# Performance work log

Measured on AMD Instinct MI355X. Metric: run time of the kernel, lower is better.

The kernel has to match this reference:

```python
import jax, jax.numpy as jnp
import numpy as np

B = 64         # number of hypernetwork samples (scenes)
N = 16384      # number of query points
SIZE_IN = 256
SIZE_H = 128
SIZE_OUT = 128


def setup_inputs() -> dict:
    key = jax.random.key(0)
    k0, k1, k2, k3, k4, k5, k6 = jax.random.split(key, 7)
    # scale weights like small init to keep activations sane
    kls0 = jax.random.normal(k0, (B, SIZE_H, SIZE_IN), dtype=jnp.float32) * 0.05
    kls1 = jax.random.normal(k1, (B, SIZE_OUT, SIZE_H), dtype=jnp.float32) * 0.05
    kls2 = jax.random.normal(k2, (B, SIZE_OUT, SIZE_IN), dtype=jnp.float32) * 0.05
    bias0 = jax.random.normal(k3, (B, SIZE_H), dtype=jnp.float32) * 0.05
    bias1 = jax.random.normal(k4, (B, SIZE_OUT), dtype=jnp.float32) * 0.05
    x = jax.random.normal(k5, (N, SIZE_IN), dtype=jnp.float32)
    batch_index = jax.random.randint(k6, (N,), 0, B, dtype=jnp.int64)
    return {
        "kls0": kls0, "kls1": kls1, "kls2": kls2,
        "bias0": bias0, "bias1": bias1,
        "x": x, "batch_index": batch_index,
    }


def reference(kls0, kls1, kls2, bias0, bias1, x, batch_index):
    bi = batch_index
    # net = F.linear(relu(x), kls0[bi], bias0[bi])  -> per-row GEMV with gathered weights
    net = jnp.einsum("nhi,ni->nh", kls0[bi], jax.nn.relu(x)) + bias0[bi]
    # dx = F.linear(relu(net), kls1[bi], bias1[bi])
    dx = jnp.einsum("noh,nh->no", kls1[bi], jax.nn.relu(net)) + bias1[bi]
    # shortcut (size_in != size_out): x_s = F.linear(x, kls2[bi])
    x_s = jnp.einsum("noi,ni->no", kls2[bi], x)
    return x_s + dx
```

## Files before the change

kernel.cpp:

```cpp
#include <hip/hip_runtime.h>

#define NSCENE 64
#define NPTS   16384
#define SIN    256
#define SH     128
#define SOUT   128
#define TILE_P 32

#define WS_PARTIAL 0
#define WS_OFFSETS 16384
#define WS_PERM    17408
#define WS_WBF16   82944
#define W0_ELEMS   (NSCENE*SH*SIN)
#define W1_ELEMS   (NSCENE*SOUT*SH)
#define W2_ELEMS   (NSCENE*SOUT*SIN)
#define WTOT       (W0_ELEMS+W1_ELEMS+W2_ELEMS)
#define CONV_BLOCKS (WTOT/2048)

typedef __attribute__((ext_vector_type(8))) short bf16x8;
typedef __attribute__((ext_vector_type(4))) float f32x4;

__device__ __forceinline__ short f2bf(float f) {
  unsigned int u = __float_as_uint(f);
  unsigned int r = (u + 0x7FFFu + ((u >> 16) & 1u)) >> 16;
  return (short)(r & 0xFFFFu);
}

__device__ __forceinline__ bf16x8 cvt8(const float* src) {
  float4 u0 = *reinterpret_cast<const float4*>(src);
  float4 u1 = *reinterpret_cast<const float4*>(src + 4);
  return (bf16x8){f2bf(u0.x), f2bf(u0.y), f2bf(u0.z), f2bf(u0.w),
                  f2bf(u1.x), f2bf(u1.y), f2bf(u1.z), f2bf(u1.w)};
}


__global__ __launch_bounds__(256) void prep_kernel(
    const int* __restrict__ bidx,
    const float* __restrict__ kls0, const float* __restrict__ kls1,
    const float* __restrict__ kls2,
    int* __restrict__ partial, short* __restrict__ wb)
{
  int b = blockIdx.x;
  int tid = threadIdx.x;
  if (b < 64) {
    __shared__ int lh[NSCENE];
    if (tid < NSCENE) lh[tid] = 0;
    __syncthreads();
    atomicAdd(&lh[bidx[b * 256 + tid]], 1);
    __syncthreads();
    if (tid < NSCENE) partial[b * 64 + tid] = lh[tid];
  } else {
    int e = ((b - 64) * 256 + tid) * 8;
    if (e < WTOT) {
      const float* src;
      if (e < W0_ELEMS) {
        int s = e >> 15, r = e & 32767;
        int w = r >> 12, ks = (r >> 9) & 7, l = (r >> 3) & 63;
        int row = w * 16 + (l & 15), k = ks * 32 + (l >> 4) * 8;
        src = kls0 + ((size_t)s << 15) + row * SIN + k;
      } else if (e < W0_ELEMS + W1_ELEMS) {
        int e1 = e - W0_ELEMS;
        int s = e1 >> 14, r = e1 & 16383;
        int w = r >> 11, ks = (r >> 9) & 3, l = (r >> 3) & 63;
        int row = w * 16 + (l & 15), k = ks * 32 + (l >> 4) * 8;
        src = kls1 + ((size_t)s << 14) + row * SH + k;
      } else {
        int e2 = e - W0_ELEMS - W1_ELEMS;
        int s = e2 >> 15, r = e2 & 32767;
        int w = r >> 12, ks = (r >> 9) & 7, l = (r >> 3) & 63;
        int row = w * 16 + (l & 15), k = ks * 32 + (l >> 4) * 8;
        src = kls2 + ((size_t)s << 15) + row * SIN + k;
      }
      *reinterpret_cast<bf16x8*>(wb + e) = cvt8(src);
    }
  }
}


__global__ __launch_bounds__(256) void scatter_kernel(
    const int* __restrict__ bidx, const int* __restrict__ partial,
    int* __restrict__ offsets, int* __restrict__ perm)
{
  __shared__ int cur[NSCENE];
  int b = blockIdx.x;
  int tid = threadIdx.x;
  if (tid < 64) {
    int s = tid;
    int colpre = 0, total = 0;
    for (int bb = 0; bb < 64; ++bb) {
      int v = partial[bb * 64 + s];
      if (bb < b) colpre += v;
      total += v;
    }
    int v = total;
    for (int off = 1; off < 64; off <<= 1) {
      int t = __shfl_up(v, off);
      if (s >= off) v += t;
    }
    int sceneoff = v - total;
    cur[s] = sceneoff + colpre;
    if (b == 0) {
      offsets[s] = sceneoff;
      if (s == 63) offsets[64] = NPTS;
    }
  }
  __syncthreads();
  int n = b * 256 + tid;
  int s = bidx[n];
  int pos = atomicAdd(&cur[s], 1);
  perm[pos] = n;
}


__global__ __launch_bounds__(512) void fused_kernel(
    const float* __restrict__ bias0, const float* __restrict__ bias1,
    const float* __restrict__ x,
    const int* __restrict__ offsets, const int* __restrict__ perm,
    const short* __restrict__ wb, float* __restrict__ out)
{
  __shared__ __align__(16) short xr[TILE_P][SIN + 8];
  __shared__ __align__(16) short xp[TILE_P][SIN + 8];
  __shared__ __align__(16) short snet[TILE_P][SH + 8];
  __shared__ int ptile[TILE_P];

  const int s    = blockIdx.x & 63;
  const int t0   = blockIdx.x >> 6;
  const int base = offsets[s];
  const int cnt  = offsets[s + 1] - base;
  const int tid  = threadIdx.x;
  const int lane = tid & 63;
  const int w    = tid >> 6;
  const int l15  = lane & 15;
  const int lh4  = lane >> 4;
  const int col  = w * 16 + l15;

  const short* B0s = wb + ((size_t)s << 15) + (w << 12) + (lane << 3);
  const short* B1s = wb + W0_ELEMS + ((size_t)s << 14) + (w << 11) + (lane << 3);
  const short* B2s = wb + W0_ELEMS + W1_ELEMS + ((size_t)s << 15) + (w << 12) + (lane << 3);

  const float bv0 = bias0[(size_t)s * SH + col];
  const float bv1 = bias1[(size_t)s * SOUT + col];

  bf16x8 b0c[8], b2c[8], b1c[4];
#pragma unroll
  for (int ks = 0; ks < 8; ++ks) {
    b0c[ks] = *reinterpret_cast<const bf16x8*>(B0s + (ks << 9));
    b2c[ks] = *reinterpret_cast<const bf16x8*>(B2s + (ks << 9));
  }
#pragma unroll
  for (int ks = 0; ks < 4; ++ks)
    b1c[ks] = *reinterpret_cast<const bf16x8*>(B1s + (ks << 9));

  for (int t = t0; t * TILE_P < cnt; t += 8) {
    __syncthreads();

    {
      int r  = tid >> 4;
      int cg = tid & 15;
      int prow = t * TILE_P + r;
      int np = (prow < cnt) ? perm[base + prow] : -1;
      if (cg == 0) ptile[r] = np;
      const float* xrow = x + (size_t)(np < 0 ? 0 : np) * SIN;
      int c0 = cg * 16;
      for (int j = 0; j < 16; j += 4) {
        float4 v = make_float4(0.f, 0.f, 0.f, 0.f);
        if (np >= 0) v = *reinterpret_cast<const float4*>(xrow + c0 + j);
        short4 p, q;
        p.x = f2bf(v.x); p.y = f2bf(v.y); p.z = f2bf(v.z); p.w = f2bf(v.w);
        q.x = f2bf(fmaxf(v.x, 0.f)); q.y = f2bf(fmaxf(v.y, 0.f));
        q.z = f2bf(fmaxf(v.z, 0.f)); q.w = f2bf(fmaxf(v.w, 0.f));
        *reinterpret_cast<short4*>(&xp[r][c0 + j]) = p;
        *reinterpret_cast<short4*>(&xr[r][c0 + j]) = q;
      }
    }
    __syncthreads();

    f32x4 acc0[2], acc[2];
#pragma unroll
    for (int mt = 0; mt < 2; ++mt) {
      acc0[mt] = (f32x4){bv0, bv0, bv0, bv0};
      acc[mt]  = (f32x4){bv1, bv1, bv1, bv1};
    }
#pragma unroll
    for (int ks = 0; ks < 8; ++ks) {
      int kc = ks * 32 + lh4 * 8;
#pragma unroll
      for (int mt = 0; mt < 2; ++mt) {
        bf16x8 aR = *reinterpret_cast<const bf16x8*>(&xr[mt * 16 + l15][kc]);
        bf16x8 aP = *reinterpret_cast<const bf16x8*>(&xp[mt * 16 + l15][kc]);
        acc0[mt] = __builtin_amdgcn_mfma_f32_16x16x32_bf16(aR, b0c[ks], acc0[mt], 0, 0, 0);
        acc[mt]  = __builtin_amdgcn_mfma_f32_16x16x32_bf16(aP, b2c[ks], acc[mt],  0, 0, 0);
      }
    }

#pragma unroll
    for (int mt = 0; mt < 2; ++mt)
#pragma unroll
      for (int r4 = 0; r4 < 4; ++r4)
        snet[mt * 16 + lh4 * 4 + r4][col] = f2bf(fmaxf(acc0[mt][r4], 0.f));
    __syncthreads();

#pragma unroll
    for (int ks = 0; ks < 4; ++ks) {
      int kc = ks * 32 + lh4 * 8;
#pragma unroll
      for (int mt = 0; mt < 2; ++mt) {
        bf16x8 aS = *reinterpret_cast<const bf16x8*>(&snet[mt * 16 + l15][kc]);
        acc[mt] = __builtin_amdgcn_mfma_f32_16x16x32_bf16(aS, b1c[ks], acc[mt], 0, 0, 0);
      }
    }

#pragma unroll
    for (int mt = 0; mt < 2; ++mt)
#pragma unroll
      for (int r4 = 0; r4 < 4; ++r4) {
        int row = mt * 16 + lh4 * 4 + r4;
        int pt = ptile[row];
        if (pt >= 0) out[(size_t)pt * SOUT + col] = acc[mt][r4];
      }
  }
}


extern "C" void kernel_launch(void* const* d_in, const int* in_sizes, int n_in,
                              void* d_out, int out_size, void* d_ws, size_t ws_size,
                              hipStream_t stream) {
  const float* kls0  = (const float*)d_in[0];
  const float* kls1  = (const float*)d_in[1];
  const float* kls2  = (const float*)d_in[2];
  const float* bias0 = (const float*)d_in[3];
  const float* bias1 = (const float*)d_in[4];
  const float* x     = (const float*)d_in[5];
  const int*   bidx  = (const int*)d_in[6];
  float* out = (float*)d_out;

  int*   partial = (int*)((char*)d_ws + WS_PARTIAL);
  int*   offsets = (int*)((char*)d_ws + WS_OFFSETS);
  int*   perm    = (int*)((char*)d_ws + WS_PERM);
  short* wb      = (short*)((char*)d_ws + WS_WBF16);

  prep_kernel<<<64 + CONV_BLOCKS, 256, 0, stream>>>(
      bidx, kls0, kls1, kls2, partial, wb);
  scatter_kernel<<<64, 256, 0, stream>>>(bidx, partial, offsets, perm);
  fused_kernel<<<512, 512, 0, stream>>>(bias0, bias1, x, offsets, perm, wb, out);
}
```

Before: 28.76 us.

## Pre-gather x into MFMA fragment layout and stream weights from global

Adds a separate gather kernel that converts x rows, in scene-sorted order padded to 32-row tiles, into bf16 fragment-ordered buffers for both the relu and raw paths. The fused kernel then reads A fragments straight from global memory instead of staging through LDS. It uses 256-thread blocks where each wave computes two column tiles, loads weight fragments per k-step rather than caching them in registers, and grows the grid to 768 blocks. The aim is to drop the LDS staging and conversion from the hot loop and raise occupancy, at the cost of an extra kernel launch and an extra round trip of x through global memory.

```diff
diff --git a/kernel.cpp b/kernel.cpp
--- a/kernel.cpp
+++ b/kernel.cpp
@@ -5,17 +5,19 @@
 #define SIN    256
 #define SH     128
 #define SOUT   128
-#define TILE_P 32
+#define XSLOTS 18432
 
 #define WS_PARTIAL 0
 #define WS_OFFSETS 16384
-#define WS_PERM    17408
-#define WS_WBF16   82944
+#define WS_SLOTMAP 17408
+#define WS_WBF16   (17408 + 73728)
+#define WS_XG      (WS_WBF16 + 10485760)
 #define W0_ELEMS   (NSCENE*SH*SIN)
 #define W1_ELEMS   (NSCENE*SOUT*SH)
 #define W2_ELEMS   (NSCENE*SOUT*SIN)
 #define WTOT       (W0_ELEMS+W1_ELEMS+W2_ELEMS)
 #define CONV_BLOCKS (WTOT/2048)
+#define XR_ELEMS   (XSLOTS * 256)
 
 typedef __attribute__((ext_vector_type(8))) short bf16x8;
 typedef __attribute__((ext_vector_type(4))) float f32x4;
@@ -55,20 +57,20 @@
       const float* src;
       if (e < W0_ELEMS) {
         int s = e >> 15, r = e & 32767;
-        int w = r >> 12, ks = (r >> 9) & 7, l = (r >> 3) & 63;
-        int row = w * 16 + (l & 15), k = ks * 32 + (l >> 4) * 8;
+        int cg = r >> 12, ks = (r >> 9) & 7, l = (r >> 3) & 63;
+        int row = cg * 16 + (l & 15), k = ks * 32 + (l >> 4) * 8;
         src = kls0 + ((size_t)s << 15) + row * SIN + k;
       } else if (e < W0_ELEMS + W1_ELEMS) {
         int e1 = e - W0_ELEMS;
         int s = e1 >> 14, r = e1 & 16383;
-        int w = r >> 11, ks = (r >> 9) & 3, l = (r >> 3) & 63;
-        int row = w * 16 + (l & 15), k = ks * 32 + (l >> 4) * 8;
+        int cg = r >> 11, ks = (r >> 9) & 3, l = (r >> 3) & 63;
+        int row = cg * 16 + (l & 15), k = ks * 32 + (l >> 4) * 8;
         src = kls1 + ((size_t)s << 14) + row * SH + k;
       } else {
         int e2 = e - W0_ELEMS - W1_ELEMS;
         int s = e2 >> 15, r = e2 & 32767;
-        int w = r >> 12, ks = (r >> 9) & 7, l = (r >> 3) & 63;
-        int row = w * 16 + (l & 15), k = ks * 32 + (l >> 4) * 8;
+        int cg = r >> 12, ks = (r >> 9) & 7, l = (r >> 3) & 63;
+        int row = cg * 16 + (l & 15), k = ks * 32 + (l >> 4) * 8;
         src = kls2 + ((size_t)s << 15) + row * SIN + k;
       }
       *reinterpret_cast<bf16x8*>(wb + e) = cvt8(src);
@@ -79,9 +81,10 @@
 
 __global__ __launch_bounds__(256) void scatter_kernel(
     const int* __restrict__ bidx, const int* __restrict__ partial,
-    int* __restrict__ offsets, int* __restrict__ perm)
+    int* __restrict__ offsets, int* __restrict__ slotmap)
 {
   __shared__ int cur[NSCENE];
+  __shared__ int scnt[NSCENE], soff[NSCENE];
   int b = blockIdx.x;
   int tid = threadIdx.x;
   if (tid < 64) {
@@ -92,121 +95,154 @@
       if (bb < b) colpre += v;
       total += v;
     }
-    int v = total;
+    int p = (total + 31) & ~31;
+    int v = p;
     for (int off = 1; off < 64; off <<= 1) {
       int t = __shfl_up(v, off);
       if (s >= off) v += t;
     }
-    int sceneoff = v - total;
-    cur[s] = sceneoff + colpre;
+    int offp = v - p;
+    cur[s]  = offp + colpre;
+    scnt[s] = total;
+    soff[s] = offp;
     if (b == 0) {
-      offsets[s] = sceneoff;
-      if (s == 63) offsets[64] = NPTS;
+      offsets[s] = offp;
+      if (s == 63) offsets[64] = v;
     }
   }
   __syncthreads();
+  if (b == 0 && tid < 64) {
+    int st = soff[tid] + scnt[tid];
+    int en = soff[tid] + ((scnt[tid] + 31) & ~31);
+    for (int i = st; i < en; ++i) slotmap[i] = -1;
+  }
   int n = b * 256 + tid;
-  int s = bidx[n];
-  int pos = atomicAdd(&cur[s], 1);
-  perm[pos] = n;
-}
-
-
-__global__ __launch_bounds__(512) void fused_kernel(
+  int s2 = bidx[n];
+  int pos = atomicAdd(&cur[s2], 1);
+  slotmap[pos] = n;
+}
+
+
+__global__ __launch_bounds__(256) void xgather_kernel(
+    const float* __restrict__ x, const int* __restrict__ slotmap,
+    short* __restrict__ xg)
+{
+  int slot = blockIdx.x * 32 + (threadIdx.x >> 3);
+  int ks   = threadIdx.x & 7;
+  int n = slotmap[slot];
+  if ((unsigned)n >= (unsigned)NPTS) return;
+  const float* px = x + (size_t)n * SIN + ks * 32;
+  size_t fo = ((size_t)(slot >> 4) << 12) + (ks << 9) + ((slot & 15) << 3);
+  short* xr = xg + fo;
+  short* xp = xg + XR_ELEMS + fo;
+#pragma unroll
+  for (int h4 = 0; h4 < 4; ++h4) {
+    float4 u0 = *reinterpret_cast<const float4*>(px + h4 * 8);
+    float4 u1 = *reinterpret_cast<const float4*>(px + h4 * 8 + 4);
+    bf16x8 vp = (bf16x8){f2bf(u0.x), f2bf(u0.y), f2bf(u0.z), f2bf(u0.w),
+                         f2bf(u1.x), f2bf(u1.y), f2bf(u1.z), f2bf(u1.w)};
+    bf16x8 vr = (bf16x8){f2bf(fmaxf(u0.x, 0.f)), f2bf(fmaxf(u0.y, 0.f)),
+                         f2bf(fmaxf(u0.z, 0.f)), f2bf(fmaxf(u0.w, 0.f)),
+                         f2bf(fmaxf(u1.x, 0.f)), f2bf(fmaxf(u1.y, 0.f)),
+                         f2bf(fmaxf(u1.z, 0.f)), f2bf(fmaxf(u1.w, 0.f))};
+    *reinterpret_cast<bf16x8*>(xp + h4 * 128) = vp;
+    *reinterpret_cast<bf16x8*>(xr + h4 * 128) = vr;
+  }
+}
+
+
+__global__ __launch_bounds__(256, 4) void fused_kernel(
     const float* __restrict__ bias0, const float* __restrict__ bias1,
-    const float* __restrict__ x,
-    const int* __restrict__ offsets, const int* __restrict__ perm,
-    const short* __restrict__ wb, float* __restrict__ out)
-{
-  __shared__ __align__(16) short xr[TILE_P][SIN + 8];
-  __shared__ __align__(16) short xp[TILE_P][SIN + 8];
-  __shared__ __align__(16) short snet[TILE_P][SH + 8];
-  __shared__ int ptile[TILE_P];
-
-  const int s    = blockIdx.x & 63;
-  const int t0   = blockIdx.x >> 6;
-  const int base = offsets[s];
-  const int cnt  = offsets[s + 1] - base;
-  const int tid  = threadIdx.x;
-  const int lane = tid & 63;
-  const int w    = tid >> 6;
-  const int l15  = lane & 15;
-  const int lh4  = lane >> 4;
-  const int col  = w * 16 + l15;
-
-  const short* B0s = wb + ((size_t)s << 15) + (w << 12) + (lane << 3);
-  const short* B1s = wb + W0_ELEMS + ((size_t)s << 14) + (w << 11) + (lane << 3);
-  const short* B2s = wb + W0_ELEMS + W1_ELEMS + ((size_t)s << 15) + (w << 12) + (lane << 3);
-
-  const float bv0 = bias0[(size_t)s * SH + col];
-  const float bv1 = bias1[(size_t)s * SOUT + col];
-
-  bf16x8 b0c[8], b2c[8], b1c[4];
-#pragma unroll
-  for (int ks = 0; ks < 8; ++ks) {
-    b0c[ks] = *reinterpret_cast<const bf16x8*>(B0s + (ks << 9));
-    b2c[ks] = *reinterpret_cast<const bf16x8*>(B2s + (ks << 9));
-  }
-#pragma unroll
-  for (int ks = 0; ks < 4; ++ks)
-    b1c[ks] = *reinterpret_cast<const bf16x8*>(B1s + (ks << 9));
-
-  for (int t = t0; t * TILE_P < cnt; t += 8) {
-    __syncthreads();
-
-    {
-      int r  = tid >> 4;
-      int cg = tid & 15;
-      int prow = t * TILE_P + r;
-      int np = (prow < cnt) ? perm[base + prow] : -1;
-      if (cg == 0) ptile[r] = np;
-      const float* xrow = x + (size_t)(np < 0 ? 0 : np) * SIN;
-      int c0 = cg * 16;
-      for (int j = 0; j < 16; j += 4) {
-        float4 v = make_float4(0.f, 0.f, 0.f, 0.f);
-        if (np >= 0) v = *reinterpret_cast<const float4*>(xrow + c0 + j);
-        short4 p, q;
-        p.x = f2bf(v.x); p.y = f2bf(v.y); p.z = f2bf(v.z); p.w = f2bf(v.w);
-        q.x = f2bf(fmaxf(v.x, 0.f)); q.y = f2bf(fmaxf(v.y, 0.f));
-        q.z = f2bf(fmaxf(v.z, 0.f)); q.w = f2bf(fmaxf(v.w, 0.f));
-        *reinterpret_cast<short4*>(&xp[r][c0 + j]) = p;
-        *reinterpret_cast<short4*>(&xr[r][c0 + j]) = q;
-      }
-    }
-    __syncthreads();
-
-    f32x4 acc0[2], acc[2];
-#pragma unroll
-    for (int mt = 0; mt < 2; ++mt) {
-      acc0[mt] = (f32x4){bv0, bv0, bv0, bv0};
-      acc[mt]  = (f32x4){bv1, bv1, bv1, bv1};
-    }
+    const int* __restrict__ offsets, const int* __restrict__ slotmap,
+    const short* __restrict__ wb, const short* __restrict__ xg,
+    float* __restrict__ out)
+{
+  __shared__ __align__(16) short snet[32][SH + 8];
+
+  const int s     = blockIdx.x & 63;
+  const int tslot = blockIdx.x >> 6;
+  const int base  = offsets[s];
+  const int cntp  = offsets[s + 1] - base;
+  const int tid   = threadIdx.x;
+  const int lane  = tid & 63;
+  const int w     = tid >> 6;
+  const int l15   = lane & 15;
+  const int lh4   = lane >> 4;
+
+  const short* wb0 = wb + ((size_t)s << 15);
+  const short* wb1 = wb + W0_ELEMS + ((size_t)s << 14);
+  const short* wb2 = wb + W0_ELEMS + W1_ELEMS + ((size_t)s << 15);
+  const short* xr  = xg;
+  const short* xp  = xg + XR_ELEMS;
+
+  float bv0[2], bv1[2];
+#pragma unroll
+  for (int nt = 0; nt < 2; ++nt) {
+    int col = (2 * w + nt) * 16 + l15;
+    bv0[nt] = bias0[(size_t)s * SH + col];
+    bv1[nt] = bias1[(size_t)s * SOUT + col];
+  }
+
+  for (int t = tslot; t * 32 < cntp; t += 12) {
+    const int p0 = base + t * 32;
+    int ptv = (lane < 32) ? slotmap[p0 + lane] : -1;
+    const size_t xo = ((size_t)(p0 >> 4) << 12) + (lane << 3);
+    __syncthreads();
+
+    f32x4 acc0[2][2], acc1[2][2];
+#pragma unroll
+    for (int mt = 0; mt < 2; ++mt)
+#pragma unroll
+      for (int nt = 0; nt < 2; ++nt) {
+        acc0[mt][nt] = (f32x4){bv0[nt], bv0[nt], bv0[nt], bv0[nt]};
+        acc1[mt][nt] = (f32x4){bv1[nt], bv1[nt], bv1[nt], bv1[nt]};
+      }
+
 #pragma unroll
     for (int ks = 0; ks < 8; ++ks) {
-      int kc = ks * 32 + lh4 * 8;
+      bf16x8 aR[2], aP[2], b0f[2], b2f[2];
 #pragma unroll
       for (int mt = 0; mt < 2; ++mt) {
-        bf16x8 aR = *reinterpret_cast<const bf16x8*>(&xr[mt * 16 + l15][kc]);
-        bf16x8 aP = *reinterpret_cast<const bf16x8*>(&xp[mt * 16 + l15][kc]);
-        acc0[mt] = __builtin_amdgcn_mfma_f32_16x16x32_bf16(aR, b0c[ks], acc0[mt], 0, 0, 0);
-        acc[mt]  = __builtin_amdgcn_mfma_f32_16x16x32_bf16(aP, b2c[ks], acc[mt],  0, 0, 0);
-      }
+        aR[mt] = *reinterpret_cast<const bf16x8*>(xr + xo + ((size_t)mt << 12) + (ks << 9));
+        aP[mt] = *reinterpret_cast<const bf16x8*>(xp + xo + ((size_t)mt << 12) + (ks << 9));
+      }
+#pragma unroll
+      for (int nt = 0; nt < 2; ++nt) {
+        int fo = ((2 * w + nt) << 12) + (ks << 9) + (lane << 3);
+        b0f[nt] = *reinterpret_cast<const bf16x8*>(wb0 + fo);
+        b2f[nt] = *reinterpret_cast<const bf16x8*>(wb2 + fo);
+      }
+#pragma unroll
+      for (int mt = 0; mt < 2; ++mt)
+#pragma unroll
+        for (int nt = 0; nt < 2; ++nt) {
+          acc0[mt][nt] = __builtin_amdgcn_mfma_f32_16x16x32_bf16(aR[mt], b0f[nt], acc0[mt][nt], 0, 0, 0);
+          acc1[mt][nt] = __builtin_amdgcn_mfma_f32_16x16x32_bf16(aP[mt], b2f[nt], acc1[mt][nt], 0, 0, 0);
+        }
     }
 
 #pragma unroll
     for (int mt = 0; mt < 2; ++mt)
 #pragma unroll
-      for (int r4 = 0; r4 < 4; ++r4)
-        snet[mt * 16 + lh4 * 4 + r4][col] = f2bf(fmaxf(acc0[mt][r4], 0.f));
+      for (int nt = 0; nt < 2; ++nt)
+#pragma unroll
+        for (int r4 = 0; r4 < 4; ++r4)
+          snet[mt * 16 + lh4 * 4 + r4][(2 * w + nt) * 16 + l15] =
+              f2bf(fmaxf(acc0[mt][nt][r4], 0.f));
     __syncthreads();
 
 #pragma unroll
     for (int ks = 0; ks < 4; ++ks) {
-      int kc = ks * 32 + lh4 * 8;
+      bf16x8 b1f[2];
+#pragma unroll
+      for (int nt = 0; nt < 2; ++nt)
+        b1f[nt] = *reinterpret_cast<const bf16x8*>(wb1 + ((2 * w + nt) << 11) + (ks << 9) + (lane << 3));
 #pragma unroll
       for (int mt = 0; mt < 2; ++mt) {
-        bf16x8 aS = *reinterpret_cast<const bf16x8*>(&snet[mt * 16 + l15][kc]);
-        acc[mt] = __builtin_amdgcn_mfma_f32_16x16x32_bf16(aS, b1c[ks], acc[mt], 0, 0, 0);
+        bf16x8 aS = *reinterpret_cast<const bf16x8*>(&snet[mt * 16 + l15][ks * 32 + lh4 * 8]);
+#pragma unroll
+        for (int nt = 0; nt < 2; ++nt)
+          acc1[mt][nt] = __builtin_amdgcn_mfma_f32_16x16x32_bf16(aS, b1f[nt], acc1[mt][nt], 0, 0, 0);
       }
     }
 
@@ -215,8 +251,12 @@
 #pragma unroll
       for (int r4 = 0; r4 < 4; ++r4) {
         int row = mt * 16 + lh4 * 4 + r4;
-        int pt = ptile[row];
-        if (pt >= 0) out[(size_t)pt * SOUT + col] = acc[mt][r4];
+        int pt = __shfl(ptv, row);
+        if (pt >= 0) {
+#pragma unroll
+          for (int nt = 0; nt < 2; ++nt)
+            out[(size_t)pt * SOUT + (2 * w + nt) * 16 + l15] = acc1[mt][nt][r4];
+        }
       }
   }
 }
@@ -236,11 +276,13 @@
 
   int*   partial = (int*)((char*)d_ws + WS_PARTIAL);
   int*   offsets = (int*)((char*)d_ws + WS_OFFSETS);
-  int*   perm    = (int*)((char*)d_ws + WS_PERM);
+  int*   slotmap = (int*)((char*)d_ws + WS_SLOTMAP);
   short* wb      = (short*)((char*)d_ws + WS_WBF16);
+  short* xg      = (short*)((char*)d_ws + WS_XG);
 
   prep_kernel<<<64 + CONV_BLOCKS, 256, 0, stream>>>(
       bidx, kls0, kls1, kls2, partial, wb);
-  scatter_kernel<<<64, 256, 0, stream>>>(bidx, partial, offsets, perm);
-  fused_kernel<<<512, 512, 0, stream>>>(bias0, bias1, x, offsets, perm, wb, out);
-}
+  scatter_kernel<<<64, 256, 0, stream>>>(bidx, partial, offsets, slotmap);
+  xgather_kernel<<<XSLOTS / 32, 256, 0, stream>>>(x, slotmap, xg);
+  fused_kernel<<<768, 256, 0, stream>>>(bias0, bias1, offsets, slotmap, wb, xg, out);
+}
```

After: 61.32 us. +113.2%, slower.

## Fuse histogram, scatter and weight conversion into one per-scene kernel

Applied to the files above, without the earlier changes.

Replaces the three-kernel pipeline (histogram plus bf16 weight pre-conversion, scatter into a permutation, compute) with a single kernel. Each block scans the whole batch_index array to build its scene's point list in shared memory with a block-wide prefix sum. It converts its scene's fp32 weights to bf16 fragments directly in registers, so the workspace round trips and two kernel launches go away. The trade-off is that every block re-reads all of batch_index, and the weights are converted redundantly by the 8 blocks per scene. The list is capped at 768 points per scene, which assumes a roughly uniform scene distribution.

```diff
diff --git a/kernel.cpp b/kernel.cpp
--- a/kernel.cpp
+++ b/kernel.cpp
@@ -5,17 +5,7 @@
 #define SIN    256
 #define SH     128
 #define SOUT   128
-#define TILE_P 32
-
-#define WS_PARTIAL 0
-#define WS_OFFSETS 16384
-#define WS_PERM    17408
-#define WS_WBF16   82944
-#define W0_ELEMS   (NSCENE*SH*SIN)
-#define W1_ELEMS   (NSCENE*SOUT*SH)
-#define W2_ELEMS   (NSCENE*SOUT*SIN)
-#define WTOT       (W0_ELEMS+W1_ELEMS+W2_ELEMS)
-#define CONV_BLOCKS (WTOT/2048)
+#define MAXP   768
 
 typedef __attribute__((ext_vector_type(8))) short bf16x8;
 typedef __attribute__((ext_vector_type(4))) float f32x4;
@@ -34,99 +24,20 @@
 }
 
 
-__global__ __launch_bounds__(256) void prep_kernel(
-    const int* __restrict__ bidx,
+__global__ __launch_bounds__(512) void fused_all(
     const float* __restrict__ kls0, const float* __restrict__ kls1,
-    const float* __restrict__ kls2,
-    int* __restrict__ partial, short* __restrict__ wb)
+    const float* __restrict__ kls2, const float* __restrict__ bias0,
+    const float* __restrict__ bias1, const float* __restrict__ x,
+    const int* __restrict__ bidx, float* __restrict__ out)
 {
-  int b = blockIdx.x;
-  int tid = threadIdx.x;
-  if (b < 64) {
-    __shared__ int lh[NSCENE];
-    if (tid < NSCENE) lh[tid] = 0;
-    __syncthreads();
-    atomicAdd(&lh[bidx[b * 256 + tid]], 1);
-    __syncthreads();
-    if (tid < NSCENE) partial[b * 64 + tid] = lh[tid];
-  } else {
-    int e = ((b - 64) * 256 + tid) * 8;
-    if (e < WTOT) {
-      const float* src;
-      if (e < W0_ELEMS) {
-        int s = e >> 15, r = e & 32767;
-        int w = r >> 12, ks = (r >> 9) & 7, l = (r >> 3) & 63;
-        int row = w * 16 + (l & 15), k = ks * 32 + (l >> 4) * 8;
-        src = kls0 + ((size_t)s << 15) + row * SIN + k;
-      } else if (e < W0_ELEMS + W1_ELEMS) {
-        int e1 = e - W0_ELEMS;
-        int s = e1 >> 14, r = e1 & 16383;
-        int w = r >> 11, ks = (r >> 9) & 3, l = (r >> 3) & 63;
-        int row = w * 16 + (l & 15), k = ks * 32 + (l >> 4) * 8;
-        src = kls1 + ((size_t)s << 14) + row * SH + k;
-      } else {
-        int e2 = e - W0_ELEMS - W1_ELEMS;
-        int s = e2 >> 15, r = e2 & 32767;
-        int w = r >> 12, ks = (r >> 9) & 7, l = (r >> 3) & 63;
-        int row = w * 16 + (l & 15), k = ks * 32 + (l >> 4) * 8;
-        src = kls2 + ((size_t)s << 15) + row * SIN + k;
-      }
-      *reinterpret_cast<bf16x8*>(wb + e) = cvt8(src);
-    }
-  }
-}
-
-
-__global__ __launch_bounds__(256) void scatter_kernel(
-    const int* __restrict__ bidx, const int* __restrict__ partial,
-    int* __restrict__ offsets, int* __restrict__ perm)
-{
-  __shared__ int cur[NSCENE];
-  int b = blockIdx.x;
-  int tid = threadIdx.x;
-  if (tid < 64) {
-    int s = tid;
-    int colpre = 0, total = 0;
-    for (int bb = 0; bb < 64; ++bb) {
-      int v = partial[bb * 64 + s];
-      if (bb < b) colpre += v;
-      total += v;
-    }
-    int v = total;
-    for (int off = 1; off < 64; off <<= 1) {
-      int t = __shfl_up(v, off);
-      if (s >= off) v += t;
-    }
-    int sceneoff = v - total;
-    cur[s] = sceneoff + colpre;
-    if (b == 0) {
-      offsets[s] = sceneoff;
-      if (s == 63) offsets[64] = NPTS;
-    }
-  }
-  __syncthreads();
-  int n = b * 256 + tid;
-  int s = bidx[n];
-  int pos = atomicAdd(&cur[s], 1);
-  perm[pos] = n;
-}
-
-
-__global__ __launch_bounds__(512) void fused_kernel(
-    const float* __restrict__ bias0, const float* __restrict__ bias1,
-    const float* __restrict__ x,
-    const int* __restrict__ offsets, const int* __restrict__ perm,
-    const short* __restrict__ wb, float* __restrict__ out)
-{
-  __shared__ __align__(16) short xr[TILE_P][SIN + 8];
-  __shared__ __align__(16) short xp[TILE_P][SIN + 8];
-  __shared__ __align__(16) short snet[TILE_P][SH + 8];
-  __shared__ int ptile[TILE_P];
+  __shared__ int   slist[MAXP];
+  __shared__ int   wsum[8], wbase[8], cnt_s;
+  __shared__ __align__(16) short xr[32][SIN + 8];
+  __shared__ __align__(16) short xp[32][SIN + 8];
+  __shared__ __align__(16) short snet[32][SH + 8];
 
   const int s    = blockIdx.x & 63;
   const int t0   = blockIdx.x >> 6;
-  const int base = offsets[s];
-  const int cnt  = offsets[s + 1] - base;
   const int tid  = threadIdx.x;
   const int lane = tid & 63;
   const int w    = tid >> 6;
@@ -134,52 +45,95 @@
   const int lh4  = lane >> 4;
   const int col  = w * 16 + l15;
 
-  const short* B0s = wb + ((size_t)s << 15) + (w << 12) + (lane << 3);
-  const short* B1s = wb + W0_ELEMS + ((size_t)s << 14) + (w << 11) + (lane << 3);
-  const short* B2s = wb + W0_ELEMS + W1_ELEMS + ((size_t)s << 15) + (w << 12) + (lane << 3);
+  int c = 0;
+  {
+    const int4* b4 = reinterpret_cast<const int4*>(bidx) + tid * 8;
+#pragma unroll
+    for (int k = 0; k < 8; ++k) {
+      int4 v = b4[k];
+      c += (v.x == s) + (v.y == s) + (v.z == s) + (v.w == s);
+    }
+  }
+  int inc = c;
+#pragma unroll
+  for (int off = 1; off < 64; off <<= 1) {
+    int t = __shfl_up(inc, off);
+    if (lane >= off) inc += t;
+  }
+  if (lane == 63) wsum[w] = inc;
+  __syncthreads();
+  if (tid < 64) {
+    int v = (lane < 8) ? wsum[lane] : 0;
+#pragma unroll
+    for (int off = 1; off < 8; off <<= 1) {
+      int t = __shfl_up(v, off);
+      if (lane >= off) v += t;
+    }
+    if (lane < 8) wbase[lane] = v - wsum[lane];
+    if (lane == 7) cnt_s = v;
+  }
+  __syncthreads();
+  {
+    int base = wbase[w] + inc - c;
+    const int4* b4 = reinterpret_cast<const int4*>(bidx) + tid * 8;
+#pragma unroll
+    for (int k = 0; k < 8; ++k) {
+      int4 v = b4[k];
+      int n = tid * 32 + k * 4;
+      if (v.x == s && base < MAXP) slist[base++] = n;
+      if (v.y == s && base < MAXP) slist[base++] = n + 1;
+      if (v.z == s && base < MAXP) slist[base++] = n + 2;
+      if (v.w == s && base < MAXP) slist[base++] = n + 3;
+    }
+  }
 
+  const float* W0r = kls0 + ((size_t)s << 15) + (size_t)col * SIN + lh4 * 8;
+  const float* W2r = kls2 + ((size_t)s << 15) + (size_t)col * SIN + lh4 * 8;
+  const float* W1r = kls1 + ((size_t)s << 14) + (size_t)col * SH + lh4 * 8;
+  bf16x8 b0c[8], b2c[8], b1c[4];
+#pragma unroll
+  for (int ks = 0; ks < 8; ++ks) {
+    b0c[ks] = cvt8(W0r + ks * 32);
+    b2c[ks] = cvt8(W2r + ks * 32);
+  }
+#pragma unroll
+  for (int ks = 0; ks < 4; ++ks)
+    b1c[ks] = cvt8(W1r + ks * 32);
   const float bv0 = bias0[(size_t)s * SH + col];
   const float bv1 = bias1[(size_t)s * SOUT + col];
 
-  bf16x8 b0c[8], b2c[8], b1c[4];
-#pragma unroll
-  for (int ks = 0; ks < 8; ++ks) {
-    b0c[ks] = *reinterpret_cast<const bf16x8*>(B0s + (ks << 9));
-    b2c[ks] = *reinterpret_cast<const bf16x8*>(B2s + (ks << 9));
-  }
-#pragma unroll
-  for (int ks = 0; ks < 4; ++ks)
-    b1c[ks] = *reinterpret_cast<const bf16x8*>(B1s + (ks << 9));
+  __syncthreads();
+  const int cnt = cnt_s;
 
-  for (int t = t0; t * TILE_P < cnt; t += 8) {
-    __syncthreads();
+  for (int t = t0; t * 32 < cnt; t += 8) {
+    if (t != t0) __syncthreads();
 
     {
       int r  = tid >> 4;
       int cg = tid & 15;
-      int prow = t * TILE_P + r;
-      int np = (prow < cnt) ? perm[base + prow] : -1;
-      if (cg == 0) ptile[r] = np;
-      const float* xrow = x + (size_t)(np < 0 ? 0 : np) * SIN;
-      int c0 = cg * 16;
+      int pr = t * 32 + r;
+      int np = (pr < cnt) ? slist[pr] : -1;
+      const float* xrow = x + (size_t)(np < 0 ? 0 : np) * SIN + cg * 16;
+#pragma unroll
       for (int j = 0; j < 16; j += 4) {
         float4 v = make_float4(0.f, 0.f, 0.f, 0.f);
-        if (np >= 0) v = *reinterpret_cast<const float4*>(xrow + c0 + j);
+        if (np >= 0) v = *reinterpret_cast<const float4*>(xrow + j);
         short4 p, q;
         p.x = f2bf(v.x); p.y = f2bf(v.y); p.z = f2bf(v.z); p.w = f2bf(v.w);
         q.x = f2bf(fmaxf(v.x, 0.f)); q.y = f2bf(fmaxf(v.y, 0.f));
         q.z = f2bf(fmaxf(v.z, 0.f)); q.w = f2bf(fmaxf(v.w, 0.f));
-        *reinterpret_cast<short4*>(&xp[r][c0 + j]) = p;
-        *reinterpret_cast<short4*>(&xr[r][c0 + j]) = q;
+        *reinterpret_cast<short4*>(&xp[r][cg * 16 + j]) = p;
+        *reinterpret_cast<short4*>(&xr[r][cg * 16 + j]) = q;
       }
     }
+    int ptv = (lane < 32 && t * 32 + lane < cnt) ? slist[t * 32 + lane] : -1;
     __syncthreads();
 
-    f32x4 acc0[2], acc[2];
+    f32x4 acc0[2], acc1[2];
 #pragma unroll
     for (int mt = 0; mt < 2; ++mt) {
       acc0[mt] = (f32x4){bv0, bv0, bv0, bv0};
-      acc[mt]  = (f32x4){bv1, bv1, bv1, bv1};
+      acc1[mt] = (f32x4){bv1, bv1, bv1, bv1};
     }
 #pragma unroll
     for (int ks = 0; ks < 8; ++ks) {
@@ -189,7 +143,7 @@
         bf16x8 aR = *reinterpret_cast<const bf16x8*>(&xr[mt * 16 + l15][kc]);
         bf16x8 aP = *reinterpret_cast<const bf16x8*>(&xp[mt * 16 + l15][kc]);
         acc0[mt] = __builtin_amdgcn_mfma_f32_16x16x32_bf16(aR, b0c[ks], acc0[mt], 0, 0, 0);
-        acc[mt]  = __builtin_amdgcn_mfma_f32_16x16x32_bf16(aP, b2c[ks], acc[mt],  0, 0, 0);
+        acc1[mt] = __builtin_amdgcn_mfma_f32_16x16x32_bf16(aP, b2c[ks], acc1[mt], 0, 0, 0);
       }
     }
 
@@ -206,7 +160,7 @@
 #pragma unroll
       for (int mt = 0; mt < 2; ++mt) {
         bf16x8 aS = *reinterpret_cast<const bf16x8*>(&snet[mt * 16 + l15][kc]);
-        acc[mt] = __builtin_amdgcn_mfma_f32_16x16x32_bf16(aS, b1c[ks], acc[mt], 0, 0, 0);
+        acc1[mt] = __builtin_amdgcn_mfma_f32_16x16x32_bf16(aS, b1c[ks], acc1[mt], 0, 0, 0);
       }
     }
 
@@ -215,8 +169,8 @@
 #pragma unroll
       for (int r4 = 0; r4 < 4; ++r4) {
         int row = mt * 16 + lh4 * 4 + r4;
-        int pt = ptile[row];
-        if (pt >= 0) out[(size_t)pt * SOUT + col] = acc[mt][r4];
+        int pt = __shfl(ptv, row);
+        if (pt >= 0) out[(size_t)pt * SOUT + col] = acc1[mt][r4];
       }
   }
 }
@@ -234,13 +188,5 @@
   const int*   bidx  = (const int*)d_in[6];
   float* out = (float*)d_out;
 
-  int*   partial = (int*)((char*)d_ws + WS_PARTIAL);
-  int*   offsets = (int*)((char*)d_ws + WS_OFFSETS);
-  int*   perm    = (int*)((char*)d_ws + WS_PERM);
-  short* wb      = (short*)((char*)d_ws + WS_WBF16);
-
-  prep_kernel<<<64 + CONV_BLOCKS, 256, 0, stream>>>(
-      bidx, kls0, kls1, kls2, partial, wb);
-  scatter_kernel<<<64, 256, 0, stream>>>(bidx, partial, offsets, perm);
-  fused_kernel<<<512, 512, 0, stream>>>(bias0, bias1, x, offsets, perm, wb, out);
+  fused_all<<<512, 512, 0, stream>>>(kls0, kls1, kls2, bias0, bias1, x, bidx, out);
 }
```

Result: slower. 45.21 us (+57.2%).
